# Performance work log

Hardware: AMD Instinct MI355X
Metric: run time of the kernel (lower is better)

Reference implementation:

```python
import jax, jax.numpy as jnp
import numpy as np

H, D = 4, 32            # heads, per-head dim
HD = H * D              # hidden_dim = output_dim = 128
ND, NG = 10000, 30000   # num disease / gene nodes
E_DG, E_GD, E_GG = 150000, 150000, 300000
L = 2                   # num HGTConv layers


def setup_inputs() -> dict:
    key = jax.random.key(0)
    ks = jax.random.split(key, 16)
    s = 0.05
    return {
        "x_d": jax.random.normal(ks[0], (ND, HD), jnp.float32),
        "x_g": jax.random.normal(ks[1], (NG, HD), jnp.float32),
        "src_dg": jax.random.randint(ks[2], (E_DG,), 0, ND),
        "dst_dg": jax.random.randint(ks[3], (E_DG,), 0, NG),
        "src_gd": jax.random.randint(ks[4], (E_GD,), 0, NG),
        "dst_gd": jax.random.randint(ks[5], (E_GD,), 0, ND),
        "src_gg": jax.random.randint(ks[6], (E_GG,), 0, NG),
        "dst_gg": jax.random.randint(ks[7], (E_GG,), 0, NG),
        # fused K/Q/V projection per node type, stacked over layers
        "Wkqv_d": jax.random.normal(ks[8], (L, HD, 3 * HD), jnp.float32) * s,
        "bkqv_d": jnp.zeros((L, 3 * HD), jnp.float32),
        "Wkqv_g": jax.random.normal(ks[9], (L, HD, 3 * HD), jnp.float32) * s,
        "bkqv_g": jnp.zeros((L, 3 * HD), jnp.float32),
        # output linear per node type
        "Wout_d": jax.random.normal(ks[10], (L, HD, HD), jnp.float32) * s,
        "bout_d": jnp.zeros((L, HD), jnp.float32),
        "Wout_g": jax.random.normal(ks[11], (L, HD, HD), jnp.float32) * s,
        "bout_g": jnp.zeros((L, HD), jnp.float32),
        # learnable skip gates per node type
        "skip_d": jnp.ones((L,), jnp.float32),
        "skip_g": jnp.ones((L,), jnp.float32),
        # per edge-type relation matrices (key, message) and priors, 3 edge types
        "arel": jax.random.normal(ks[12], (L, 3, H, D, D), jnp.float32) * s,
        "mrel": jax.random.normal(ks[13], (L, 3, H, D, D), jnp.float32) * s,
        "prel": jnp.ones((L, 3, H), jnp.float32),
    }


def _hgt_forward(x_d, x_g, src_dg, dst_dg, src_gd, dst_gd, src_gg, dst_gg,
                 Wkqv_d, bkqv_d, Wkqv_g, bkqv_g, Wout_d, bout_d, Wout_g, bout_g,
                 skip_d, skip_g, arel, mrel, prel):
    scale = 1.0 / (D ** 0.5)
    for l in range(L):
        def kqv(x, W, b):
            t = (x @ W + b).reshape(-1, 3, H, D)
            return t[:, 0], t[:, 1], t[:, 2]

        k_d, q_d, v_d = kqv(x_d, Wkqv_d[l], bkqv_d[l])
        k_g, q_g, v_g = kqv(x_g, Wkqv_g[l], bkqv_g[l])

        def edge_msgs(k_src, v_src, q_dst, src, dst, et):
            # gather src K/V, transform by per-edge-type relation matrices
            ke = jnp.einsum('ehd,hdf->ehf', k_src[src], arel[l, et])  # [E,H,D]
            ve = jnp.einsum('ehd,hdf->ehf', v_src[src], mrel[l, et])  # [E,H,D]
            a = jnp.sum(q_dst[dst] * ke, axis=-1) * prel[l, et] * scale  # [E,H]
            return a, ve

        a_dg, v_dg = edge_msgs(k_d, v_d, q_g, src_dg, dst_dg, 0)
        a_gd, v_gd = edge_msgs(k_g, v_g, q_d, src_gd, dst_gd, 1)
        a_gg, v_gg = edge_msgs(k_g, v_g, q_g, src_gg, dst_gg, 2)

        def aggregate(alphas, vals, dsts, n):
            # segment softmax over ALL incoming edges of a dst node (across edge types)
            a = jnp.concatenate(alphas, axis=0)
            v = jnp.concatenate(vals, axis=0)
            d = jnp.concatenate(dsts, axis=0)
            amax = jax.ops.segment_max(a, d, num_segments=n)
            ex = jnp.exp(a - amax[d])
            den = jax.ops.segment_sum(ex, d, num_segments=n)
            w = ex / den[d]
            out = jax.ops.segment_sum(w[:, :, None] * v, d, num_segments=n)
            return out.reshape(n, HD)

        agg_g = aggregate([a_dg, a_gg], [v_dg, v_gg], [dst_dg, dst_gg], NG)
        agg_d = aggregate([a_gd], [v_gd], [dst_gd], ND)

        def update(agg, x, Wout, bout, skip):
            o = jax.nn.gelu(agg) @ Wout + bout
            g = jax.nn.sigmoid(skip)
            return g * o + (1.0 - g) * x

        x_d = update(agg_d, x_d, Wout_d[l], bout_d[l], skip_d[l])
        x_g = update(agg_g, x_g, Wout_g[l], bout_g[l], skip_g[l])
    return x_d, x_g


def reference(x_d, x_g, src_dg, dst_dg, src_gd, dst_gd, src_gg, dst_gg,
              Wkqv_d, bkqv_d, Wkqv_g, bkqv_g, Wout_d, bout_d, Wout_g, bout_g,
              skip_d, skip_g, arel, mrel, prel):
    return _hgt_forward(x_d, x_g, src_dg, dst_dg, src_gd, dst_gd, src_gg, dst_gg,
                        Wkqv_d, bkqv_d, Wkqv_g, bkqv_g, Wout_d, bout_d, Wout_g, bout_g,
                        skip_d, skip_g, arel, mrel, prel)
```

## Files before the change

### kernel.cpp

```cpp
#include <hip/hip_runtime.h>
#include <hip/hip_bf16.h>

#define H 4
#define D 32
#define HD 128
#define ND 10000
#define NG 30000
#define E_DG 150000
#define E_GD 150000
#define E_GG 300000
#define NE (E_DG + E_GD + E_GG)
#define EG (E_DG + E_GG)
#define NLAYER 2
#define NBG 30
#define NBD 10
#define OCG 640
#define OCD 384
#define GOFF ((size_t)ND * OCD)
#define NSCAT 2344
#define NGEMM 5625

typedef _Float16 f16;
typedef __attribute__((ext_vector_type(2))) _Float16 f16x2;
typedef __attribute__((ext_vector_type(8))) _Float16 f16x8;
typedef __attribute__((ext_vector_type(8))) unsigned short u16x8;
typedef __attribute__((ext_vector_type(4))) float f32x4;

__device__ __forceinline__ float bu(unsigned short u) {
    return __uint_as_float(((unsigned)u) << 16);
}
__device__ __forceinline__ float ldraw(const void* p, size_t i, bool isf32) {
    return isf32 ? ((const float*)p)[i] : bu(((const unsigned short*)p)[i]);
}
__device__ __forceinline__ float gelu(float v) {
    const float c = 0.79788456080286536f * (v + 0.044715f * v * v * v);
    return 0.5f * v * (1.0f + tanhf(c));
}

__device__ __forceinline__ void combine_one(
    int idx, int GENE, bool isf32,
    const void* W, const void* bvec,
    const void* arel, const void* mrel, const void* prel,
    f16* __restrict__ Wp, float* __restrict__ bp) {
    const int OC = GENE ? OCG : OCD;
    const int l = idx / (OC * 128);
    const int rem = idx - l * OC * 128;
    const int col = rem >> 7;
    const int d = rem & 127;
    const int g = col >> 7;
    const int jj = col & 127;
    const int h = jj >> 5, f = jj & 31;
    const size_t wbase = (size_t)l * 128 * 384;
    const size_t bbase = (size_t)l * 384;
    float val, bv = 0.f;
    if (g == 0) {
        val = ldraw(W, wbase + d * 384 + 128 + jj, isf32);
        bv = ldraw(bvec, bbase + 128 + jj, isf32);
    } else {
        const int et = GENE ? ((g <= 2) ? 1 : 2) : 0;
        const bool isk = (g & 1);
        const void* mat = isk ? arel : mrel;
        const size_t mbase = (((size_t)(l * 3 + et) * H + h) << 10) + f;
        const int sb = isk ? 0 : 256;
        val = 0.f;
        for (int dd = 0; dd < 32; dd++)
            val += ldraw(W, wbase + d * 384 + sb + h * 32 + dd, isf32) *
                   ldraw(mat, mbase + dd * 32, isf32);
        if (d == 0)
            for (int dd = 0; dd < 32; dd++)
                bv += ldraw(bvec, bbase + sb + h * 32 + dd, isf32) *
                      ldraw(mat, mbase + dd * 32, isf32);
        if (isk) {
            const float sc = ldraw(prel, (size_t)(l * 3 + et) * H + h, isf32) *
                             (0.17677669529663689f * 1.4426950408889634f);
            val *= sc;
            bv *= sc;
        }
    }
    Wp[(size_t)l * 4 * OC * 32 + ((size_t)(d >> 5) * OC + col) * 32 + (d & 31)] = (f16)val;
    if (d == 0) bp[l * OC + col] = bv;
}

__global__ __launch_bounds__(256) void k_prep0(
    const void* x0,
    const void* wkqvd_r, const void* bkqvd_r,
    const void* wkqvg_r, const void* bkqvg_r,
    const void* arel_r, const void* mrel_r, const void* prel_r,
    const void* woutd_r, const void* woutg_r,
    const void* boutd_r, const void* boutg_r,
    const void* skipd_r, const void* skipg_r,
    f16* __restrict__ Wp_d, float* __restrict__ bp_d,
    f16* __restrict__ Wp_g, float* __restrict__ bp_g,
    f16* __restrict__ Wpod, f16* __restrict__ Wpog,
    float* __restrict__ boutc_d, float* __restrict__ boutc_g,
    float* __restrict__ gates, int* __restrict__ flag,
    int* __restrict__ cnt, int* __restrict__ ready) {
    const int tid = threadIdx.x;
    __shared__ int sbad;
    if (tid == 0) sbad = 0;
    __syncthreads();
    {
        const unsigned short* xs = (const unsigned short*)x0;
        int bad = 0;
        for (int i = tid; i < 1024; i += 256)
            if (!(fabsf(bu(xs[i])) < 1e6f)) bad = 1;
        if (bad) sbad = 1;
    }
    __syncthreads();
    const bool isf32 = (sbad != 0);

    const int b = blockIdx.x;
    if (b < 1280) {
        int idx = b * 256 + tid;
        const int nd = NLAYER * OCD * 128;
        const int ng = NLAYER * OCG * 128;
        const int np = 2 * NLAYER * 128 * 128;
        if (idx < nd) {
            combine_one(idx, 0, isf32, wkqvd_r, bkqvd_r, arel_r, mrel_r, prel_r, Wp_d, bp_d);
        } else if ((idx -= nd) < ng) {
            combine_one(idx, 1, isf32, wkqvg_r, bkqvg_r, arel_r, mrel_r, prel_r, Wp_g, bp_g);
        } else if ((idx -= ng) < np) {
            const int type = idx >= NLAYER * 128 * 128;
            int rem = idx - type * NLAYER * 128 * 128;
            const int l = rem / (128 * 128);
            rem -= l * 128 * 128;
            const int d = rem >> 7, col = rem & 127;
            const float w = ldraw(type ? woutg_r : woutd_r,
                                  (size_t)l * 128 * 128 + d * 128 + col, isf32);
            f16* out = (type ? Wpog : Wpod) +
                ((size_t)l * 4 + (d >> 5)) * 128 * 32 + col * 32 + (d & 31);
            *out = (f16)w;
        }
    } else if (b == 1280) {
        if (tid < NBG + NBD) ready[tid] = 0;
        if (tid == 0) {
            flag[0] = isf32 ? 1 : 0;
            gates[0] = 1.f / (1.f + expf(-ldraw(skipd_r, 0, isf32)));
            gates[1] = 1.f / (1.f + expf(-ldraw(skipg_r, 0, isf32)));
            gates[2] = 1.f / (1.f + expf(-ldraw(skipd_r, 1, isf32)));
            gates[3] = 1.f / (1.f + expf(-ldraw(skipg_r, 1, isf32)));
        }
        for (int i = tid; i < NLAYER * 128; i += 256) {
            boutc_d[i] = ldraw(boutd_r, i, isf32);
            boutc_g[i] = ldraw(boutg_r, i, isf32);
        }
    } else {
        const int base = (b - 1281) * 1000;
        for (int i = tid; i < 1000; i += 256) cnt[base + i] = 0;
    }
}

__global__ __launch_bounds__(256) void k_hist(
    const int* __restrict__ dst_dg, const int* __restrict__ dst_gg,
    const int* __restrict__ dst_gd,
    int* __restrict__ cnt_g, int* __restrict__ cnt_d) {
    const int i = blockIdx.x * 256 + threadIdx.x;
    if (i < E_DG) atomicAdd(cnt_g + dst_dg[i], 1);
    else if (i < EG) atomicAdd(cnt_g + dst_gg[i - E_DG], 1);
    else if (i < NE) atomicAdd(cnt_d + dst_gd[i - EG], 1);
}

__global__ __launch_bounds__(256) void k_scan(
    const int* __restrict__ cnt_g, const int* __restrict__ cnt_d,
    int* __restrict__ ready,
    int* __restrict__ rp_g, int* __restrict__ cur_g,
    int* __restrict__ rp_d, int* __restrict__ cur_d) {
    const int b = blockIdx.x;
    const int tid = threadIdx.x;
    const bool isg = (b < NBG);
    const int* cnt = isg ? cnt_g : cnt_d;
    int* rp = isg ? rp_g : rp_d;
    int* cur = isg ? cur_g : cur_d;
    const int n = isg ? NG : ND;
    const int lb = isg ? b : (b - NBG);
    const int i0 = lb * 1024 + tid * 4;
    int v[4];
    int t = 0;
#pragma unroll
    for (int j = 0; j < 4; j++) {
        v[j] = (i0 + j < n) ? cnt[i0 + j] : 0;
        t += v[j];
    }
    __shared__ int sdata[256];
    __shared__ int red2[256];
    __shared__ int s_off;
    sdata[tid] = t;
    __syncthreads();
    for (int d = 1; d < 256; d <<= 1) {
        const int u = (tid >= d) ? sdata[tid - d] : 0;
        __syncthreads();
        sdata[tid] += u;
        __syncthreads();
    }
    const int total = sdata[255];
    if (tid == 0) atomicExch(&ready[b], total + 1);
    const int p0 = isg ? 0 : NBG;
    const int npred = b - p0;
    int part = 0;
    for (int i = tid; i < npred; i += 256) {
        int vv;
        do { vv = atomicAdd(&ready[p0 + i], 0); } while (vv == 0);
        part += vv - 1;
    }
    red2[tid] = part;
    __syncthreads();
    for (int d = 128; d > 0; d >>= 1) {
        if (tid < d) red2[tid] += red2[tid + d];
        __syncthreads();
    }
    if (tid == 0) s_off = red2[0];
    __syncthreads();
    int run = s_off + sdata[tid] - t;
#pragma unroll
    for (int j = 0; j < 4; j++) {
        if (i0 + j < n) {
            cur[i0 + j] = run;
            run += v[j];
            rp[i0 + j + 1] = run;
        }
    }
    if (tid == 0 && lb == 0) rp[0] = 0;
}

__global__ __launch_bounds__(256) void k_scatter_gemm0(
    const int* __restrict__ src_dg, const int* __restrict__ dst_dg,
    const int* __restrict__ src_gg, const int* __restrict__ dst_gg,
    const int* __restrict__ src_gd, const int* __restrict__ dst_gd,
    int* __restrict__ cur_g, int* __restrict__ cur_d,
    int* __restrict__ edges_g, int* __restrict__ edges_d,
    const void* xd_r, const void* xg_r, const int* __restrict__ flag,
    const f16* __restrict__ Wpd, const float* __restrict__ bpd,
    const f16* __restrict__ Wpg, const float* __restrict__ bpg,
    f16* __restrict__ tab) {
    if (blockIdx.x < NSCAT) {
        const int i = blockIdx.x * 256 + threadIdx.x;
        if (i < E_DG) {
            const int pos = atomicAdd(cur_g + dst_dg[i], 1);
            edges_g[pos] = src_dg[i] * OCD + 128;
        } else if (i < EG) {
            const int j = i - E_DG;
            const int pos = atomicAdd(cur_g + dst_gg[j], 1);
            edges_g[pos] = (int)GOFF + src_gg[j] * OCG + 384;
        } else if (i < NE) {
            const int j = i - EG;
            const int pos = atomicAdd(cur_d + dst_gd[j], 1);
            edges_d[pos] = (int)GOFF + src_gd[j] * OCG + 128;
        }
        return;
    }
    const bool isf32 = (*flag != 0);
    int w = (blockIdx.x - NSCAT) * 4 + (threadIdx.x >> 6);
    const void* xr;
    const f16* Wp;
    const float* bias;
    f16* out;
    int mt, nt, OC;
    if (w < 3750) {
        xr = xd_r; Wp = Wpd; bias = bpd; out = tab; OC = OCD;
        nt = w / 625; mt = w - nt * 625;
    } else {
        w -= 3750;
        xr = xg_r; Wp = Wpg; bias = bpg; out = tab + GOFF; OC = OCG;
        nt = w / 1875; mt = w - nt * 1875;
    }
    const int lane = threadIdx.x & 63;
    const int r = lane & 15, q4 = lane >> 4;
    const int node0 = mt << 4, col0 = nt << 6;
    f32x4 acc0 = {0.f, 0.f, 0.f, 0.f};
    f32x4 acc1 = acc0, acc2 = acc0, acc3 = acc0;
#pragma unroll
    for (int kb = 0; kb < 4; kb++) {
        f16x8 a;
        const size_t base = (size_t)(node0 + r) * 128 + kb * 32 + q4 * 8;
        if (isf32) {
            const float* xp = (const float*)xr + base;
            const float4 u0 = *(const float4*)xp;
            const float4 u1 = *(const float4*)(xp + 4);
            a[0] = (f16)u0.x; a[1] = (f16)u0.y; a[2] = (f16)u0.z; a[3] = (f16)u0.w;
            a[4] = (f16)u1.x; a[5] = (f16)u1.y; a[6] = (f16)u1.z; a[7] = (f16)u1.w;
        } else {
            const u16x8 u = *(const u16x8*)((const unsigned short*)xr + base);
#pragma unroll
            for (int i = 0; i < 8; i++) a[i] = (f16)bu(u[i]);
        }
        const f16* wb = Wp + ((size_t)kb * OC + col0 + r) * 32 + q4 * 8;
        const f16x8 b0 = *(const f16x8*)(wb);
        const f16x8 b1 = *(const f16x8*)(wb + 512);
        const f16x8 b2 = *(const f16x8*)(wb + 1024);
        const f16x8 b3 = *(const f16x8*)(wb + 1536);
        acc0 = __builtin_amdgcn_mfma_f32_16x16x32_f16(a, b0, acc0, 0, 0, 0);
        acc1 = __builtin_amdgcn_mfma_f32_16x16x32_f16(a, b1, acc1, 0, 0, 0);
        acc2 = __builtin_amdgcn_mfma_f32_16x16x32_f16(a, b2, acc2, 0, 0, 0);
        acc3 = __builtin_amdgcn_mfma_f32_16x16x32_f16(a, b3, acc3, 0, 0, 0);
    }
    const f32x4 accs[4] = {acc0, acc1, acc2, acc3};
#pragma unroll
    for (int t = 0; t < 4; t++) {
        const int col = col0 + t * 16 + r;
        const float bb = bias[col];
#pragma unroll
        for (int reg = 0; reg < 4; reg++)
            out[(size_t)(node0 + q4 * 4 + reg) * OC + col] = (f16)(accs[t][reg] + bb);
    }
}

__global__ __launch_bounds__(256) void k_agg(
    const int* __restrict__ rp_g, const int* __restrict__ edges_g,
    const int* __restrict__ rp_d, const int* __restrict__ edges_d,
    const f16* __restrict__ tab, f16* __restrict__ gagg) {
    const int wid = blockIdx.x * 4 + (threadIdx.x >> 6);
    const int lane = threadIdx.x & 63;
    const int slot = lane >> 4, sub = lane & 15;

    int node, row;
    const int *rp, *edges;
    size_t qoff;
    if (wid < NG) {
        node = wid; rp = rp_g; edges = edges_g;
        qoff = GOFF + (size_t)node * OCG;
        row = ND + node;
    } else {
        node = wid - NG; rp = rp_d; edges = edges_d;
        qoff = (size_t)node * OCD;
        row = node;
    }

    union U { f16x8 v; f16x2 p[4]; };
    U q;
    q.v = *(const f16x8*)(tab + qoff + sub * 8);

    float m = -1e30f, s = 0.f;
    float acc[8];
#pragma unroll
    for (int i = 0; i < 8; i++) acc[i] = 0.f;

    const int r0 = rp[node], r1 = rp[node + 1];
    int e = r0 + slot;

    auto kvload = [&](int rec, U& k, U& v) {
        const f16* p = tab + (size_t)rec + sub * 8;
        k.v = *(const f16x8*)p;
        v.v = *(const f16x8*)(p + 128);
    };

    int recA0 = (e < r1) ? edges[e] : 0;
    int recB0 = (e + 4 < r1) ? edges[e + 4] : 0;
    U kA0, vA0, kB0, vB0;
    kvload(recA0, kA0, vA0);
    kvload(recB0, kB0, vB0);
    int recA1 = (e + 8 < r1) ? edges[e + 8] : 0;
    int recB1 = (e + 12 < r1) ? edges[e + 12] : 0;

    while (e < r1) {
        const int recA2 = (e + 16 < r1) ? edges[e + 16] : 0;
        const int recB2 = (e + 20 < r1) ? edges[e + 20] : 0;
        U kA1, vA1, kB1, vB1;
        kvload(recA1, kA1, vA1);
        kvload(recB1, kB1, vB1);

        float pA = __builtin_amdgcn_fdot2(q.p[0], kA0.p[0], 0.f, false);
        float pB = __builtin_amdgcn_fdot2(q.p[0], kB0.p[0], 0.f, false);
        pA = __builtin_amdgcn_fdot2(q.p[1], kA0.p[1], pA, false);
        pB = __builtin_amdgcn_fdot2(q.p[1], kB0.p[1], pB, false);
        pA = __builtin_amdgcn_fdot2(q.p[2], kA0.p[2], pA, false);
        pB = __builtin_amdgcn_fdot2(q.p[2], kB0.p[2], pB, false);
        pA = __builtin_amdgcn_fdot2(q.p[3], kA0.p[3], pA, false);
        pB = __builtin_amdgcn_fdot2(q.p[3], kB0.p[3], pB, false);
        pA += __shfl_xor(pA, 1);
        pB += __shfl_xor(pB, 1);
        pA += __shfl_xor(pA, 2);
        pB += __shfl_xor(pB, 2);
        const float aA = pA;
        const float aB = (e + 4 < r1) ? pB : -1e30f;
        const float mn = fmaxf(m, fmaxf(aA, aB));
        const float c = exp2f(m - mn);
        const float eaA = exp2f(aA - mn);
        const float eaB = exp2f(aB - mn);
        s = s * c + eaA + eaB;
#pragma unroll
        for (int i = 0; i < 8; i++)
            acc[i] = fmaf(eaB, (float)vB0.v[i], fmaf(eaA, (float)vA0.v[i], acc[i] * c));
        m = mn;
        recA0 = recA1; recB0 = recB1; recA1 = recA2; recB1 = recB2;
        kA0 = kA1; vA0 = vA1; kB0 = kB1; vB0 = vB1;
        e += 8;
    }

#pragma unroll
    for (int mask = 16; mask <= 32; mask <<= 1) {
        const float m2 = __shfl_xor(m, mask);
        const float s2 = __shfl_xor(s, mask);
        const float M = fmaxf(m, m2);
        const float c1 = exp2f(m - M);
        const float c2 = exp2f(m2 - M);
        s = s * c1 + s2 * c2;
#pragma unroll
        for (int i = 0; i < 8; i++) {
            const float o = __shfl_xor(acc[i], mask);
            acc[i] = acc[i] * c1 + o * c2;
        }
        m = M;
    }

    const float inv = (s > 0.f) ? (1.f / s) : 0.f;
    if (slot == 0) {
        f16x8 o;
#pragma unroll
        for (int i = 0; i < 8; i++) o[i] = (f16)gelu(acc[i] * inv);
        *(f16x8*)(gagg + (size_t)row * HD + sub * 8) = o;
    }
}

__global__ __launch_bounds__(256) void k_updgemm(
    const f16* __restrict__ gagg,
    const f16* __restrict__ Wpod0, const f16* __restrict__ Wpog0,
    const float* __restrict__ boutc_d0, const float* __restrict__ boutc_g0,
    const float* __restrict__ gates,
    const void* xd_r, const void* xg_r, const int* __restrict__ flag,
    f16* __restrict__ xball,
    const f16* __restrict__ Wpd1, const float* __restrict__ bpd1,
    const f16* __restrict__ Wpg1, const float* __restrict__ bpg1,
    f16* __restrict__ tab) {
    __shared__ f16 xls[32 * 128];
    const bool isf32 = (*flag != 0);
    const int tid = threadIdx.x;
    const int wv = tid >> 6, lane = tid & 63;
    const int r = lane & 15, q4 = lane >> 4;

    {
        const int mtl = wv >> 1, nt = wv & 1;
        const int mtile = blockIdx.x * 2 + mtl;
        const int node0 = mtile * 16;
        const bool gene = (node0 >= ND);
        const f16* Wp = gene ? Wpog0 : Wpod0;
        const float* bias = gene ? boutc_g0 : boutc_d0;
        const float g = gates[gene ? 1 : 0];
        const int col0 = nt << 6;
        f32x4 acc0 = {0.f, 0.f, 0.f, 0.f};
        f32x4 acc1 = acc0, acc2 = acc0, acc3 = acc0;
#pragma unroll
        for (int kb = 0; kb < 4; kb++) {
            const f16x8 a = *(const f16x8*)(gagg + (size_t)(node0 + r) * 128 + kb * 32 + q4 * 8);
            const f16* wb = Wp + ((size_t)kb * 128 + col0 + r) * 32 + q4 * 8;
            const f16x8 b0 = *(const f16x8*)(wb);
            const f16x8 b1 = *(const f16x8*)(wb + 512);
            const f16x8 b2 = *(const f16x8*)(wb + 1024);
            const f16x8 b3 = *(const f16x8*)(wb + 1536);
            acc0 = __builtin_amdgcn_mfma_f32_16x16x32_f16(a, b0, acc0, 0, 0, 0);
            acc1 = __builtin_amdgcn_mfma_f32_16x16x32_f16(a, b1, acc1, 0, 0, 0);
            acc2 = __builtin_amdgcn_mfma_f32_16x16x32_f16(a, b2, acc2, 0, 0, 0);
            acc3 = __builtin_amdgcn_mfma_f32_16x16x32_f16(a, b3, acc3, 0, 0, 0);
        }
        const f32x4 accs[4] = {acc0, acc1, acc2, acc3};
        const void* xr = gene ? xg_r : xd_r;
        const int lrow0 = node0 - (gene ? ND : 0);
#pragma unroll
        for (int t = 0; t < 4; t++) {
            const int col = col0 + t * 16 + r;
            const float bb = bias[col];
#pragma unroll
            for (int reg = 0; reg < 4; reg++) {
                const int rr = q4 * 4 + reg;
                const float xo = ldraw(xr, (size_t)(lrow0 + rr) * 128 + col, isf32);
                const float xn = g * (accs[t][reg] + bb) + (1.f - g) * xo;
                xls[(mtl * 16 + rr) * 128 + col] = (f16)xn;
                xball[(size_t)(node0 + rr) * 128 + col] = (f16)xn;
            }
        }
    }
    __syncthreads();

    const int mt0 = blockIdx.x * 2;
    const int n0 = ((mt0 * 16) >= ND) ? 10 : 6;
    const int n1 = (((mt0 + 1) * 16) >= ND) ? 10 : 6;
    for (int it = wv; it < n0 + n1; it += 4) {
        const int mtl = (it < n0) ? 0 : 1;
        const int ntl = (it < n0) ? it : (it - n0);
        const int node0 = (mt0 + mtl) * 16;
        const bool gene = (node0 >= ND);
        const int OC = gene ? OCG : OCD;
        const f16* Wp = gene ? Wpg1 : Wpd1;
        const float* bias = gene ? bpg1 : bpd1;
        f16* out = gene ? (tab + GOFF) : tab;
        const int trow0 = node0 - (gene ? ND : 0);
        const int col0 = ntl << 6;
        f32x4 acc0 = {0.f, 0.f, 0.f, 0.f};
        f32x4 acc1 = acc0, acc2 = acc0, acc3 = acc0;
#pragma unroll
        for (int kb = 0; kb < 4; kb++) {
            const f16x8 a = *(const f16x8*)(xls + (mtl * 16 + r) * 128 + kb * 32 + q4 * 8);
            const f16* wb = Wp + ((size_t)kb * OC + col0 + r) * 32 + q4 * 8;
            const f16x8 b0 = *(const f16x8*)(wb);
            const f16x8 b1 = *(const f16x8*)(wb + 512);
            const f16x8 b2 = *(const f16x8*)(wb + 1024);
            const f16x8 b3 = *(const f16x8*)(wb + 1536);
            acc0 = __builtin_amdgcn_mfma_f32_16x16x32_f16(a, b0, acc0, 0, 0, 0);
            acc1 = __builtin_amdgcn_mfma_f32_16x16x32_f16(a, b1, acc1, 0, 0, 0);
            acc2 = __builtin_amdgcn_mfma_f32_16x16x32_f16(a, b2, acc2, 0, 0, 0);
            acc3 = __builtin_amdgcn_mfma_f32_16x16x32_f16(a, b3, acc3, 0, 0, 0);
        }
        const f32x4 accs[4] = {acc0, acc1, acc2, acc3};
#pragma unroll
        for (int t = 0; t < 4; t++) {
            const int col = col0 + t * 16 + r;
            const float bb = bias[col];
#pragma unroll
            for (int reg = 0; reg < 4; reg++)
                out[(size_t)(trow0 + q4 * 4 + reg) * OC + col] = (f16)(accs[t][reg] + bb);
        }
    }
}

__global__ __launch_bounds__(256) void k_upd1(
    const f16* __restrict__ gagg,
    const f16* __restrict__ Wpod1, const f16* __restrict__ Wpog1,
    const float* __restrict__ boutc_d1, const float* __restrict__ boutc_g1,
    const float* __restrict__ gates,
    const f16* __restrict__ xball, float* __restrict__ dout) {
    const int w = blockIdx.x * 4 + (threadIdx.x >> 6);
    const int nt = w / 2500, mt = w - nt * 2500;
    const int node0 = mt << 4;
    const bool gene = (node0 >= ND);
    const f16* Wp = gene ? Wpog1 : Wpod1;
    const float* bias = gene ? boutc_g1 : boutc_d1;
    const float g = gates[gene ? 1 : 0];
    const int lane = threadIdx.x & 63;
    const int r = lane & 15, q4 = lane >> 4;
    const int col0 = nt << 6;
    f32x4 acc0 = {0.f, 0.f, 0.f, 0.f};
    f32x4 acc1 = acc0, acc2 = acc0, acc3 = acc0;
#pragma unroll
    for (int kb = 0; kb < 4; kb++) {
        const f16x8 a = *(const f16x8*)(gagg + (size_t)(node0 + r) * 128 + kb * 32 + q4 * 8);
        const f16* wb = Wp + ((size_t)kb * 128 + col0 + r) * 32 + q4 * 8;
        const f16x8 b0 = *(const f16x8*)(wb);
        const f16x8 b1 = *(const f16x8*)(wb + 512);
        const f16x8 b2 = *(const f16x8*)(wb + 1024);
        const f16x8 b3 = *(const f16x8*)(wb + 1536);
        acc0 = __builtin_amdgcn_mfma_f32_16x16x32_f16(a, b0, acc0, 0, 0, 0);
        acc1 = __builtin_amdgcn_mfma_f32_16x16x32_f16(a, b1, acc1, 0, 0, 0);
        acc2 = __builtin_amdgcn_mfma_f32_16x16x32_f16(a, b2, acc2, 0, 0, 0);
        acc3 = __builtin_amdgcn_mfma_f32_16x16x32_f16(a, b3, acc3, 0, 0, 0);
    }
    const f32x4 accs[4] = {acc0, acc1, acc2, acc3};
#pragma unroll
    for (int t = 0; t < 4; t++) {
        const int col = col0 + t * 16 + r;
        const float bb = bias[col];
#pragma unroll
        for (int reg = 0; reg < 4; reg++) {
            const size_t idx = (size_t)(node0 + q4 * 4 + reg) * 128 + col;
            dout[idx] = g * (accs[t][reg] + bb) + (1.f - g) * (float)xball[idx];
        }
    }
}

static inline size_t alignup(size_t v) { return (v + 15) & ~(size_t)15; }

extern "C" void kernel_launch(void* const* d_in, const int* in_sizes, int n_in,
                              void* d_out, int out_size, void* d_ws, size_t ws_size,
                              hipStream_t stream) {
    (void)in_sizes; (void)n_in; (void)out_size; (void)ws_size;
    const int* src_dg = (const int*)d_in[2];
    const int* dst_dg = (const int*)d_in[3];
    const int* src_gd = (const int*)d_in[4];
    const int* dst_gd = (const int*)d_in[5];
    const int* src_gg = (const int*)d_in[6];
    const int* dst_gg = (const int*)d_in[7];

    float* ws = (float*)d_ws;
    int* flag = (int*)ws; ws += 16;
    int* cnt_g  = (int*)ws; ws += alignup(NG);
    int* cnt_d  = (int*)ws; ws += alignup(ND);
    int* rp_g   = (int*)ws; ws += alignup(NG + 1);
    int* rp_d   = (int*)ws; ws += alignup(ND + 1);
    int* cur_g  = (int*)ws; ws += alignup(NG);
    int* cur_d  = (int*)ws; ws += alignup(ND);
    int* ready  = (int*)ws; ws += 64;
    int* edges_g = (int*)ws; ws += alignup(EG);
    int* edges_d = (int*)ws; ws += alignup(E_GD);
    float* bp_d = ws; ws += alignup((size_t)NLAYER * OCD);
    float* bp_g = ws; ws += alignup((size_t)NLAYER * OCG);
    float* boutc_d = ws; ws += alignup((size_t)NLAYER * 128);
    float* boutc_g = ws; ws += alignup((size_t)NLAYER * 128);
    float* gates = ws; ws += 16;
    f16* Wp_d = (f16*)ws; ws += alignup((size_t)NLAYER * 4 * OCD * 32 / 2);
    f16* Wp_g = (f16*)ws; ws += alignup((size_t)NLAYER * 4 * OCG * 32 / 2);
    f16* Wpod = (f16*)ws; ws += alignup((size_t)NLAYER * 4 * 128 * 32 / 2);
    f16* Wpog = (f16*)ws; ws += alignup((size_t)NLAYER * 4 * 128 * 32 / 2);
    f16* xball = (f16*)ws; ws += alignup((size_t)(ND + NG) * HD / 2);
    f16* gagg  = (f16*)ws; ws += alignup((size_t)(ND + NG) * HD / 2);
    f16* tab   = (f16*)ws; ws += alignup(((size_t)ND * OCD + (size_t)NG * OCG) / 2);

    k_prep0<<<1321, 256, 0, stream>>>(
        d_in[0],
        d_in[8], d_in[9], d_in[10], d_in[11],
        d_in[18], d_in[19], d_in[20],
        d_in[12], d_in[14], d_in[13], d_in[15], d_in[16], d_in[17],
        Wp_d, bp_d, Wp_g, bp_g, Wpod, Wpog, boutc_d, boutc_g,
        gates, flag, cnt_g, ready);
    k_hist<<<NSCAT, 256, 0, stream>>>(dst_dg, dst_gg, dst_gd, cnt_g, cnt_d);
    k_scan<<<NBG + NBD, 256, 0, stream>>>(cnt_g, cnt_d, ready, rp_g, cur_g, rp_d, cur_d);
    k_scatter_gemm0<<<NSCAT + NGEMM, 256, 0, stream>>>(
        src_dg, dst_dg, src_gg, dst_gg, src_gd, dst_gd,
        cur_g, cur_d, edges_g, edges_d,
        d_in[0], d_in[1], flag,
        Wp_d, bp_d, Wp_g, bp_g, tab);
    k_agg<<<(NG + ND) / 4, 256, 0, stream>>>(rp_g, edges_g, rp_d, edges_d, tab, gagg);
    k_updgemm<<<(ND + NG) / 32, 256, 0, stream>>>(
        gagg, Wpod, Wpog, boutc_d, boutc_g, gates,
        d_in[0], d_in[1], flag, xball,
        Wp_d + (size_t)4 * OCD * 32, bp_d + OCD,
        Wp_g + (size_t)4 * OCG * 32, bp_g + OCG, tab);
    k_agg<<<(NG + ND) / 4, 256, 0, stream>>>(rp_g, edges_g, rp_d, edges_d, tab, gagg);
    k_upd1<<<(ND + NG) / 32, 256, 0, stream>>>(
        gagg, Wpod + (size_t)4 * 128 * 32, Wpog + (size_t)4 * 128 * 32,
        boutc_d + 128, boutc_g + 128, gates + 2, xball, (float*)d_out);
}
```

Baseline: 372.9 us.

## Stage layer-0 GEMM inputs in LDS, pad LDS rows, drop online-softmax max tracking

```diff
diff --git a/kernel.cpp b/kernel.cpp
--- a/kernel.cpp
+++ b/kernel.cpp
@@ -18,7 +18,8 @@
 #define OCD 384
 #define GOFF ((size_t)ND * OCD)
 #define NSCAT 2344
-#define NGEMM 5625
+#define NGEMM0 1250
+#define XLSTRIDE 136
 
 typedef _Float16 f16;
 typedef __attribute__((ext_vector_type(2))) _Float16 f16x2;
@@ -232,6 +233,7 @@
     const f16* __restrict__ Wpd, const float* __restrict__ bpd,
     const f16* __restrict__ Wpg, const float* __restrict__ bpg,
     f16* __restrict__ tab) {
+    __shared__ f16 xls[32 * XLSTRIDE];
     if (blockIdx.x < NSCAT) {
         const int i = blockIdx.x * 256 + threadIdx.x;
         if (i < E_DG) {
@@ -249,58 +251,66 @@
         return;
     }
     const bool isf32 = (*flag != 0);
-    int w = (blockIdx.x - NSCAT) * 4 + (threadIdx.x >> 6);
-    const void* xr;
-    const f16* Wp;
-    const float* bias;
-    f16* out;
-    int mt, nt, OC;
-    if (w < 3750) {
-        xr = xd_r; Wp = Wpd; bias = bpd; out = tab; OC = OCD;
-        nt = w / 625; mt = w - nt * 625;
-    } else {
-        w -= 3750;
-        xr = xg_r; Wp = Wpg; bias = bpg; out = tab + GOFF; OC = OCG;
-        nt = w / 1875; mt = w - nt * 1875;
-    }
-    const int lane = threadIdx.x & 63;
+    const int tid = threadIdx.x;
+    const int mt0 = (blockIdx.x - NSCAT) * 2;
+    for (int i = tid; i < 1024; i += 256) {
+        const int row = i >> 5;
+        const int c4 = (i & 31) * 4;
+        const int gnode = mt0 * 16 + row;
+        const bool gene = (gnode >= ND);
+        const void* xr = gene ? xg_r : xd_r;
+        const size_t base = (size_t)(gene ? gnode - ND : gnode) * 128 + c4;
+        float4 v;
+        if (isf32) {
+            v = *(const float4*)((const float*)xr + base);
+        } else {
+            const ushort4 u = *(const ushort4*)((const unsigned short*)xr + base);
+            v = make_float4(bu(u.x), bu(u.y), bu(u.z), bu(u.w));
+        }
+        f16* dst = xls + row * XLSTRIDE + c4;
+        dst[0] = (f16)v.x; dst[1] = (f16)v.y; dst[2] = (f16)v.z; dst[3] = (f16)v.w;
+    }
+    __syncthreads();
+
+    const int wv = tid >> 6, lane = tid & 63;
     const int r = lane & 15, q4 = lane >> 4;
-    const int node0 = mt << 4, col0 = nt << 6;
-    f32x4 acc0 = {0.f, 0.f, 0.f, 0.f};
-    f32x4 acc1 = acc0, acc2 = acc0, acc3 = acc0;
-#pragma unroll
-    for (int kb = 0; kb < 4; kb++) {
-        f16x8 a;
-        const size_t base = (size_t)(node0 + r) * 128 + kb * 32 + q4 * 8;
-        if (isf32) {
-            const float* xp = (const float*)xr + base;
-            const float4 u0 = *(const float4*)xp;
-            const float4 u1 = *(const float4*)(xp + 4);
-            a[0] = (f16)u0.x; a[1] = (f16)u0.y; a[2] = (f16)u0.z; a[3] = (f16)u0.w;
-            a[4] = (f16)u1.x; a[5] = (f16)u1.y; a[6] = (f16)u1.z; a[7] = (f16)u1.w;
-        } else {
-            const u16x8 u = *(const u16x8*)((const unsigned short*)xr + base);
-#pragma unroll
-            for (int i = 0; i < 8; i++) a[i] = (f16)bu(u[i]);
-        }
-        const f16* wb = Wp + ((size_t)kb * OC + col0 + r) * 32 + q4 * 8;
-        const f16x8 b0 = *(const f16x8*)(wb);
-        const f16x8 b1 = *(const f16x8*)(wb + 512);
-        const f16x8 b2 = *(const f16x8*)(wb + 1024);
-        const f16x8 b3 = *(const f16x8*)(wb + 1536);
-        acc0 = __builtin_amdgcn_mfma_f32_16x16x32_f16(a, b0, acc0, 0, 0, 0);
-        acc1 = __builtin_amdgcn_mfma_f32_16x16x32_f16(a, b1, acc1, 0, 0, 0);
-        acc2 = __builtin_amdgcn_mfma_f32_16x16x32_f16(a, b2, acc2, 0, 0, 0);
-        acc3 = __builtin_amdgcn_mfma_f32_16x16x32_f16(a, b3, acc3, 0, 0, 0);
-    }
-    const f32x4 accs[4] = {acc0, acc1, acc2, acc3};
-#pragma unroll
-    for (int t = 0; t < 4; t++) {
-        const int col = col0 + t * 16 + r;
-        const float bb = bias[col];
-#pragma unroll
-        for (int reg = 0; reg < 4; reg++)
-            out[(size_t)(node0 + q4 * 4 + reg) * OC + col] = (f16)(accs[t][reg] + bb);
+    const int n0 = (mt0 * 16 >= ND) ? 10 : 6;
+    const int n1 = ((mt0 + 1) * 16 >= ND) ? 10 : 6;
+    for (int it = wv; it < n0 + n1; it += 4) {
+        const int mtl = (it < n0) ? 0 : 1;
+        const int ntl = (it < n0) ? it : (it - n0);
+        const int node0 = (mt0 + mtl) * 16;
+        const bool gene = (node0 >= ND);
+        const int OC = gene ? OCG : OCD;
+        const f16* Wp = gene ? Wpg : Wpd;
+        const float* bias = gene ? bpg : bpd;
+        f16* out = gene ? (tab + GOFF) : tab;
+        const int trow0 = node0 - (gene ? ND : 0);
+        const int col0 = ntl << 6;
+        f32x4 acc0 = {0.f, 0.f, 0.f, 0.f};
+        f32x4 acc1 = acc0, acc2 = acc0, acc3 = acc0;
+#pragma unroll
+        for (int kb = 0; kb < 4; kb++) {
+            const f16x8 a = *(const f16x8*)(xls + (mtl * 16 + r) * XLSTRIDE + kb * 32 + q4 * 8);
+            const f16* wb = Wp + ((size_t)kb * OC + col0 + r) * 32 + q4 * 8;
+            const f16x8 b0 = *(const f16x8*)(wb);
+            const f16x8 b1 = *(const f16x8*)(wb + 512);
+            const f16x8 b2 = *(const f16x8*)(wb + 1024);
+            const f16x8 b3 = *(const f16x8*)(wb + 1536);
+            acc0 = __builtin_amdgcn_mfma_f32_16x16x32_f16(a, b0, acc0, 0, 0, 0);
+            acc1 = __builtin_amdgcn_mfma_f32_16x16x32_f16(a, b1, acc1, 0, 0, 0);
+            acc2 = __builtin_amdgcn_mfma_f32_16x16x32_f16(a, b2, acc2, 0, 0, 0);
+            acc3 = __builtin_amdgcn_mfma_f32_16x16x32_f16(a, b3, acc3, 0, 0, 0);
+        }
+        const f32x4 accs[4] = {acc0, acc1, acc2, acc3};
+#pragma unroll
+        for (int t = 0; t < 4; t++) {
+            const int col = col0 + t * 16 + r;
+            const float bb = bias[col];
+#pragma unroll
+            for (int reg = 0; reg < 4; reg++)
+                out[(size_t)(trow0 + q4 * 4 + reg) * OC + col] = (f16)(accs[t][reg] + bb);
+        }
     }
 }
 
@@ -329,7 +339,7 @@
     U q;
     q.v = *(const f16x8*)(tab + qoff + sub * 8);
 
-    float m = -1e30f, s = 0.f;
+    float s = 0.f;
     float acc[8];
 #pragma unroll
     for (int i = 0; i < 8; i++) acc[i] = 0.f;
@@ -370,17 +380,12 @@
         pB += __shfl_xor(pB, 1);
         pA += __shfl_xor(pA, 2);
         pB += __shfl_xor(pB, 2);
-        const float aA = pA;
-        const float aB = (e + 4 < r1) ? pB : -1e30f;
-        const float mn = fmaxf(m, fmaxf(aA, aB));
-        const float c = exp2f(m - mn);
-        const float eaA = exp2f(aA - mn);
-        const float eaB = exp2f(aB - mn);
-        s = s * c + eaA + eaB;
+        const float eaA = exp2f(pA);
+        const float eaB = (e + 4 < r1) ? exp2f(pB) : 0.f;
+        s += eaA + eaB;
 #pragma unroll
         for (int i = 0; i < 8; i++)
-            acc[i] = fmaf(eaB, (float)vB0.v[i], fmaf(eaA, (float)vA0.v[i], acc[i] * c));
-        m = mn;
+            acc[i] = fmaf(eaB, (float)vB0.v[i], fmaf(eaA, (float)vA0.v[i], acc[i]));
         recA0 = recA1; recB0 = recB1; recA1 = recA2; recB1 = recB2;
         kA0 = kA1; vA0 = vA1; kB0 = kB1; vB0 = vB1;
         e += 8;
@@ -388,18 +393,9 @@
 
 #pragma unroll
     for (int mask = 16; mask <= 32; mask <<= 1) {
-        const float m2 = __shfl_xor(m, mask);
-        const float s2 = __shfl_xor(s, mask);
-        const float M = fmaxf(m, m2);
-        const float c1 = exp2f(m - M);
-        const float c2 = exp2f(m2 - M);
-        s = s * c1 + s2 * c2;
-#pragma unroll
-        for (int i = 0; i < 8; i++) {
-            const float o = __shfl_xor(acc[i], mask);
-            acc[i] = acc[i] * c1 + o * c2;
-        }
-        m = M;
+        s += __shfl_xor(s, mask);
+#pragma unroll
+        for (int i = 0; i < 8; i++) acc[i] += __shfl_xor(acc[i], mask);
     }
 
     const float inv = (s > 0.f) ? (1.f / s) : 0.f;
@@ -421,7 +417,7 @@
     const f16* __restrict__ Wpd1, const float* __restrict__ bpd1,
     const f16* __restrict__ Wpg1, const float* __restrict__ bpg1,
     f16* __restrict__ tab) {
-    __shared__ f16 xls[32 * 128];
+    __shared__ f16 xls[32 * XLSTRIDE];
     const bool isf32 = (*flag != 0);
     const int tid = threadIdx.x;
     const int wv = tid >> 6, lane = tid & 63;
@@ -463,7 +459,7 @@
                 const int rr = q4 * 4 + reg;
                 const float xo = ldraw(xr, (size_t)(lrow0 + rr) * 128 + col, isf32);
                 const float xn = g * (accs[t][reg] + bb) + (1.f - g) * xo;
-                xls[(mtl * 16 + rr) * 128 + col] = (f16)xn;
+                xls[(mtl * 16 + rr) * XLSTRIDE + col] = (f16)xn;
                 xball[(size_t)(node0 + rr) * 128 + col] = (f16)xn;
             }
         }
@@ -488,7 +484,7 @@
         f32x4 acc1 = acc0, acc2 = acc0, acc3 = acc0;
 #pragma unroll
         for (int kb = 0; kb < 4; kb++) {
-            const f16x8 a = *(const f16x8*)(xls + (mtl * 16 + r) * 128 + kb * 32 + q4 * 8);
+            const f16x8 a = *(const f16x8*)(xls + (mtl * 16 + r) * XLSTRIDE + kb * 32 + q4 * 8);
             const f16* wb = Wp + ((size_t)kb * OC + col0 + r) * 32 + q4 * 8;
             const f16x8 b0 = *(const f16x8*)(wb);
             const f16x8 b1 = *(const f16x8*)(wb + 512);
@@ -601,7 +597,7 @@
         gates, flag, cnt_g, ready);
     k_hist<<<NSCAT, 256, 0, stream>>>(dst_dg, dst_gg, dst_gd, cnt_g, cnt_d);
     k_scan<<<NBG + NBD, 256, 0, stream>>>(cnt_g, cnt_d, ready, rp_g, cur_g, rp_d, cur_d);
-    k_scatter_gemm0<<<NSCAT + NGEMM, 256, 0, stream>>>(
+    k_scatter_gemm0<<<NSCAT + NGEMM0, 256, 0, stream>>>(
         src_dg, dst_dg, src_gg, dst_gg, src_gd, dst_gd,
         cur_g, cur_d, edges_g, edges_d,
         d_in[0], d_in[1], flag,
```

After: 362.1 us. -2.9%, faster.
